# Kernel tuning notes

Hardware: AMD Instinct MI355X
Metric: run time of the kernel (lower is better)

The kernel has to match this reference:

```python
import jax, jax.numpy as jnp
import numpy as np
from jax import lax

V_PATCH = (1, 4, 16, 64, 256, 1024)  # must end at L
RESI = 0.5    # quant_resi ratio inside Phi
BETA = 0.25
K_PHI = 4     # share_quant_resi


def _phi_indices():
    # PhiPartiallyShared tick lookup, resolved statically per scale
    K = K_PHI
    ticks = np.linspace(1/3/K, 1 - 1/3/K, K) if K == 4 else np.linspace(1/2/K, 1 - 1/2/K, K)
    SN = len(V_PATCH)
    return [int(np.argmin(np.abs(ticks - (si / (SN - 1) if SN > 1 else 0.0)))) for si in range(SN)]


def interp_linear(x, Lo):
    # torch F.interpolate(mode='linear', align_corners=False) on last axis of [B,C,Li]
    Li = x.shape[-1]
    if Li == Lo:
        return x
    pos = (jnp.arange(Lo, dtype=jnp.float32) + 0.5) * (Li / Lo) - 0.5
    pos = jnp.clip(pos, 0.0, Li - 1)
    lo = jnp.floor(pos).astype(jnp.int32)
    hi = jnp.minimum(lo + 1, Li - 1)
    w = pos - lo.astype(jnp.float32)
    return x[..., lo] * (1.0 - w) + x[..., hi] * w


def phi_apply(h, w, b):
    # Phi: h*(1-r) + Conv1d(ks=3,pad=1)(h)*r
    y = lax.conv_general_dilated(h, w, (1,), [(1, 1)], dimension_numbers=('NCH', 'OIH', 'NCH'))
    y = y + b[None, :, None]
    return h * (1.0 - RESI) + y * RESI


def reference(f_BCL, emb, phi_w, phi_b):
    f = f_BCL.astype(jnp.float32)
    B, C, L = f.shape
    f_ng = lax.stop_gradient(f)
    f_rest = f_ng
    f_hat = jnp.zeros_like(f_ng)
    SN = len(V_PATCH)
    pidx = _phi_indices()
    e_sq = jnp.sum(emb * emb, axis=1)  # [V]
    loss = jnp.float32(0.0)
    for si, pl in enumerate(V_PATCH):
        rest = interp_linear(f_rest, pl) if si != SN - 1 else f_rest
        z = rest.transpose(0, 2, 1).reshape(-1, C)              # [B*pl, C]
        d = jnp.sum(z * z, axis=1, keepdims=True) + e_sq - 2.0 * (z @ emb.T)  # [B*pl, V]
        idx = jnp.argmin(d, axis=1)
        h = emb[idx].reshape(B, pl, C).transpose(0, 2, 1)        # [B,C,pl]
        if si != SN - 1:
            h = interp_linear(h, L)
        h = phi_apply(h, phi_w[pidx[si]], phi_b[pidx[si]])
        f_hat = f_hat + h
        f_rest = f_rest - h
        loss = loss + BETA * jnp.mean((lax.stop_gradient(f_hat) - f) ** 2) \
                    + jnp.mean((f_hat - f_ng) ** 2)
    loss = loss / SN
    # straight-through estimator
    f_hat_st = lax.stop_gradient(f_hat) - f_ng + f
    return f_hat_st, loss


def setup_inputs() -> dict:
    key = jax.random.key(0)
    k1, k2, k3 = jax.random.split(key, 3)
    B, C, L, V = 32, 32, 1024, 4096
    f_BCL = jax.random.normal(k1, (B, C, L), dtype=jnp.float32)
    emb = jax.random.normal(k2, (V, C), dtype=jnp.float32)
    phi_w = jax.random.normal(k3, (K_PHI, C, C, 3), dtype=jnp.float32) * 0.05
    phi_b = jnp.zeros((K_PHI, C), dtype=jnp.float32)
    return {"f_BCL": f_BCL, "emb": emb, "phi_w": phi_w, "phi_b": phi_b}
```

## Files before the change

kernel.cpp:

```cpp
#include <hip/hip_runtime.h>
#include <stdint.h>

#define BDIM 32
#define CDIM 32
#define LDIM 1024
#define VDIM 4096
#define BCL (BDIM*CDIM*LDIM)

typedef _Float16 f16x8 __attribute__((ext_vector_type(8)));
typedef float f32x4 __attribute__((ext_vector_type(4)));

#define PIN_V(x) asm volatile("" : "+v"(x))

__global__ void init_kernel(const float* __restrict__ f, const float* __restrict__ emb,
                            float* __restrict__ f_rest, float* __restrict__ f_hat,
                            float* __restrict__ e_sq,
                            _Float16* __restrict__ eh, _Float16* __restrict__ el,
                            float* __restrict__ loss_acc, unsigned* __restrict__ done_ctr,
                            unsigned long long* __restrict__ keys, int nkeys) {
    int i = blockIdx.x * blockDim.x + threadIdx.x;
    if (i < BCL) { f_rest[i] = f[i]; f_hat[i] = 0.0f; }
    if (i < VDIM) {
        const float* e = emb + (size_t)i * CDIM;
        float s = 0.f;
#pragma unroll
        for (int k = 0; k < 32; ++k) {
            float v = e[k];
            s = fmaf(v, v, s);
            if (eh) {
                _Float16 h = (_Float16)v;
                float r = v - (float)h;
                eh[(size_t)i*32 + k] = (_Float16)(-2.0f) * h;
                el[(size_t)i*32 + k] = (_Float16)(-2.0f) * (_Float16)r;
            }
        }
        e_sq[i] = s;
    }
    if (i < nkeys) keys[i] = ~0ull;
    if (i == 0) { *loss_acc = 0.f; *done_ctr = 0u; }
}

__global__ __launch_bounds__(256) void vq_mfma(
    const _Float16* __restrict__ z_hi, const _Float16* __restrict__ z_lo,
    const _Float16* __restrict__ e_hi, const _Float16* __restrict__ e_lo,
    const float* __restrict__ e_sq, unsigned long long* __restrict__ keys,
    int NQ, int VC, int vchunks, int vsub)
{
    const int t = threadIdx.x;
    const int lane = t & 63;
    const int w = t >> 6;
    const int qg = blockIdx.x / vchunks;
    const int vc = blockIdx.x % vchunks;
    const int vb0 = vc * (vsub * VC);

    __shared__ __align__(16) _Float16 eh_ls[256*32];
    __shared__ __align__(16) _Float16 el_ls[256*32];
    __shared__ float esq_ls[256];

    const int fr = lane & 15;
    const int kq = lane >> 4;
    const int qbase = qg*256 + w*64;
    f16x8 ah[4], al[4];
#pragma unroll
    for (int tq = 0; tq < 4; ++tq) {
        int q = qbase + tq*16 + fr;
        ah[tq] = *(const f16x8*)(z_hi + (size_t)q*32 + kq*8);
        al[tq] = *(const f16x8*)(z_lo + (size_t)q*32 + kq*8);
    }

    float bd[4][4]; int bv[4][4];
#pragma unroll
    for (int tq = 0; tq < 4; ++tq)
#pragma unroll
        for (int i = 0; i < 4; ++i) { bd[tq][i] = 3.4e38f; bv[tq][i] = 0; }

    for (int sub = 0; sub < vsub; ++sub) {
        const int vb = vb0 + sub * VC;

        {
            const float4* sH = (const float4*)(e_hi + (size_t)vb*32);
            const float4* sL = (const float4*)(e_lo + (size_t)vb*32);
            float4* dH = (float4*)eh_ls; float4* dL = (float4*)el_ls;
            int n4 = VC * 4;
            for (int x = t; x < n4; x += 256) {
                int row = x >> 2, c = x & 3;
                int ds = row*4 + (c ^ ((row >> 1) & 3));
                dH[ds] = sH[x]; dL[ds] = sL[x];
            }
            for (int v = t; v < VC; v += 256) esq_ls[v] = e_sq[vb + v];
        }
        __syncthreads();

        for (int vt = 0; vt < VC; vt += 16) {
            const int row = vt + fr;
            const int koff = (kq ^ ((row >> 1) & 3)) * 8;
            const f16x8 bh = *(const f16x8*)(eh_ls + (size_t)row*32 + koff);
            const f16x8 bl = *(const f16x8*)(el_ls + (size_t)row*32 + koff);
            float es = esq_ls[row];
            int vg = vb + row;
#pragma unroll
            for (int tq = 0; tq < 4; ++tq) {
                f32x4 acc = {es, es, es, es};
                acc = __builtin_amdgcn_mfma_f32_16x16x32_f16(ah[tq], bh, acc, 0,0,0);
                acc = __builtin_amdgcn_mfma_f32_16x16x32_f16(ah[tq], bl, acc, 0,0,0);
                acc = __builtin_amdgcn_mfma_f32_16x16x32_f16(al[tq], bh, acc, 0,0,0);
#pragma unroll
                for (int i = 0; i < 4; ++i)
                    if (acc[i] < bd[tq][i]) { bd[tq][i] = acc[i]; bv[tq][i] = vg; }
            }
        }
        __syncthreads();
    }

#pragma unroll
    for (int tq = 0; tq < 4; ++tq) {
#pragma unroll
        for (int i = 0; i < 4; ++i) {
            unsigned u = __float_as_uint(bd[tq][i]);
            u = (u & 0x80000000u) ? ~u : (u | 0x80000000u);
            unsigned long long k = ((unsigned long long)u << 32) | (unsigned)bv[tq][i];
#pragma unroll
            for (int m = 1; m < 16; m <<= 1) {
                unsigned long long o = __shfl_xor(k, m, 64); if (o < k) k = o;
            }
            if (fr == 0) {
                int q = qbase + tq*16 + kq*4 + i;
                atomicMin(&keys[q], k);
            }
        }
    }
}

__global__ __launch_bounds__(256) void vq_scan(
    const float* __restrict__ f_rest, const float* __restrict__ z_buf,
    const float* __restrict__ emb, const float* __restrict__ e_sq,
    unsigned long long* __restrict__ keys,
    int lpl, int s, int NQ, int VC, int vchunks)
{
    const int pl = 1 << lpl;
    const int t  = threadIdx.x;
    const int qg = blockIdx.x / vchunks;
    const int vc = blockIdx.x % vchunks;
    const int vb = vc * VC;

    __shared__ __align__(16) float e_ls[128 * 32];
    __shared__ float esq_ls[128];

    {
        const float4* src = (const float4*)emb + (size_t)vb * 8;
        float4* dst = (float4*)e_ls;
        for (int x = t; x < VC * 8; x += 256) dst[x] = src[x];
        if (t < VC) esq_ls[t] = e_sq[vb + t];
    }

    const int q0 = qg * 512 + t;
    const int q1 = q0 + 256;
    const int qc0 = (q0 < NQ) ? q0 : NQ - 1;
    const int qc1 = (q1 < NQ) ? q1 : NQ - 1;

    float z0[32], z1[32];
    if (z_buf) {
        const float4* p0 = (const float4*)(z_buf + (size_t)qc0 * 32);
        const float4* p1 = (const float4*)(z_buf + (size_t)qc1 * 32);
#pragma unroll
        for (int c4 = 0; c4 < 8; ++c4) {
            float4 a = p0[c4], b = p1[c4];
            z0[c4*4+0] = a.x; z0[c4*4+1] = a.y; z0[c4*4+2] = a.z; z0[c4*4+3] = a.w;
            z1[c4*4+0] = b.x; z1[c4*4+1] = b.y; z1[c4*4+2] = b.z; z1[c4*4+3] = b.w;
        }
    } else {
        int b0 = qc0 >> lpl, j0 = qc0 & (pl - 1);
        int b1 = qc1 >> lpl, j1 = qc1 & (pl - 1);
        if (pl == LDIM) {
            const float* p0 = f_rest + b0 * (CDIM * LDIM) + j0;
            const float* p1 = f_rest + b1 * (CDIM * LDIM) + j1;
#pragma unroll
            for (int c = 0; c < 32; ++c) { z0[c] = p0[c * LDIM]; z1[c] = p1[c * LDIM]; }
        } else {
            int col0 = j0 * s + (s >> 1) - 1;
            int col1 = j1 * s + (s >> 1) - 1;
            const float* p0 = f_rest + b0 * (CDIM * LDIM) + col0;
            const float* p1 = f_rest + b1 * (CDIM * LDIM) + col1;
#pragma unroll
            for (int c = 0; c < 32; ++c) {
                z0[c] = 0.5f * (p0[c * LDIM] + p0[c * LDIM + 1]);
                z1[c] = 0.5f * (p1[c * LDIM] + p1[c * LDIM + 1]);
            }
        }
    }

    __syncthreads();

    float bd0 = 3.4e38f, bd1 = 3.4e38f;
    int bv0 = 0, bv1 = 0;

#pragma unroll 1
    for (int v = 0; v < VC; v += 2) {
#pragma unroll
        for (int c = 0; c < 32; ++c) { PIN_V(z0[c]); PIN_V(z1[c]); }

        const float4* er0 = (const float4*)&e_ls[(size_t)v * 32];
        const float4* er1 = er0 + 8;
        float es0 = esq_ls[v];
        float es1 = esq_ls[v + 1];

        float4 e0 = er0[0], e1 = er1[0];
        float a00 = z0[0] * e0.x,        a01 = z0[0] * e1.x;
        float a10 = z1[0] * e0.x,        a11 = z1[0] * e1.x;
        a00 = fmaf(z0[1], e0.y, a00);    a01 = fmaf(z0[1], e1.y, a01);
        a10 = fmaf(z1[1], e0.y, a10);    a11 = fmaf(z1[1], e1.y, a11);
        a00 = fmaf(z0[2], e0.z, a00);    a01 = fmaf(z0[2], e1.z, a01);
        a10 = fmaf(z1[2], e0.z, a10);    a11 = fmaf(z1[2], e1.z, a11);
        a00 = fmaf(z0[3], e0.w, a00);    a01 = fmaf(z0[3], e1.w, a01);
        a10 = fmaf(z1[3], e0.w, a10);    a11 = fmaf(z1[3], e1.w, a11);
#pragma unroll
        for (int c4 = 1; c4 < 8; ++c4) {
            e0 = er0[c4]; e1 = er1[c4];
            a00 = fmaf(z0[c4*4+0], e0.x, a00);  a01 = fmaf(z0[c4*4+0], e1.x, a01);
            a10 = fmaf(z1[c4*4+0], e0.x, a10);  a11 = fmaf(z1[c4*4+0], e1.x, a11);
            a00 = fmaf(z0[c4*4+1], e0.y, a00);  a01 = fmaf(z0[c4*4+1], e1.y, a01);
            a10 = fmaf(z1[c4*4+1], e0.y, a10);  a11 = fmaf(z1[c4*4+1], e1.y, a11);
            a00 = fmaf(z0[c4*4+2], e0.z, a00);  a01 = fmaf(z0[c4*4+2], e1.z, a01);
            a10 = fmaf(z1[c4*4+2], e0.z, a10);  a11 = fmaf(z1[c4*4+2], e1.z, a11);
            a00 = fmaf(z0[c4*4+3], e0.w, a00);  a01 = fmaf(z0[c4*4+3], e1.w, a01);
            a10 = fmaf(z1[c4*4+3], e0.w, a10);  a11 = fmaf(z1[c4*4+3], e1.w, a11);
        }
        float d00 = fmaf(a00, -2.0f, es0);
        float d01 = fmaf(a01, -2.0f, es1);
        float d10 = fmaf(a10, -2.0f, es0);
        float d11 = fmaf(a11, -2.0f, es1);
        if (d00 < bd0) { bd0 = d00; bv0 = vb + v; }
        if (d01 < bd0) { bd0 = d01; bv0 = vb + v + 1; }
        if (d10 < bd1) { bd1 = d10; bv1 = vb + v; }
        if (d11 < bd1) { bd1 = d11; bv1 = vb + v + 1; }
    }

    if (q0 < NQ) {
        unsigned ud = __float_as_uint(bd0);
        ud = (ud & 0x80000000u) ? ~ud : (ud | 0x80000000u);
        atomicMin(&keys[q0], ((unsigned long long)ud << 32) | (unsigned)bv0);
    }
    if (q1 < NQ) {
        unsigned ud = __float_as_uint(bd1);
        ud = (ud & 0x80000000u) ? ~ud : (ud | 0x80000000u);
        atomicMin(&keys[q1], ((unsigned long long)ud << 32) | (unsigned)bv1);
    }
}

__global__ __launch_bounds__(256) void fuse_kernel(
    const float* __restrict__ f, const float* __restrict__ emb,
    const unsigned long long* __restrict__ keys,
    unsigned long long* __restrict__ keys_next, int nq_next,
    _Float16* __restrict__ zh_next, _Float16* __restrict__ zl_next, int s_next,
    const float* __restrict__ w, const float* __restrict__ bias,
    float* __restrict__ f_rest, float* __restrict__ f_hat,
    float* __restrict__ loss_acc, unsigned* __restrict__ done_ctr,
    float* __restrict__ out_loss, int pl)
{
    const int t  = threadIdx.x;
    const int b  = blockIdx.y;
    const int l0 = blockIdx.x * 64;

    if (keys_next) {
        int x = (b * gridDim.x + blockIdx.x) * 256 + t;
        if (x < nq_next) keys_next[x] = ~0ull;
    }

    __shared__ float w_s[3072];
    __shared__ float b_s[32];
    __shared__ float hs[32 * 68];
    __shared__ float red[4];

    for (int x = t; x < 3072; x += 256) w_s[x] = w[x];
    if (t < 32) b_s[t] = bias[t];

    if (t < 66) {
        int l = l0 - 1 + t;
        if (l < 0 || l >= LDIM) {
#pragma unroll
            for (int i = 0; i < 32; ++i) hs[i * 68 + t] = 0.f;
        } else {
            int lo, hi; float wg;
            if (pl == LDIM) { lo = l; hi = l; wg = 0.f; }
            else {
                float pos = (l + 0.5f) * ((float)pl / 1024.0f) - 0.5f;
                pos = fminf(fmaxf(pos, 0.f), (float)(pl - 1));
                lo = (int)floorf(pos);
                hi = min(lo + 1, pl - 1);
                wg = pos - (float)lo;
            }
            int v0 = (int)(keys[b * pl + lo] & 0xFFFFFFFFull);
            int v1 = (int)(keys[b * pl + hi] & 0xFFFFFFFFull);
            const float4* e0 = (const float4*)(emb + (size_t)v0 * 32);
            const float4* e1 = (const float4*)(emb + (size_t)v1 * 32);
            float om = 1.0f - wg;
#pragma unroll
            for (int i4 = 0; i4 < 8; ++i4) {
                float4 a = e0[i4]; float4 c = e1[i4];
                hs[(i4*4+0) * 68 + t] = a.x * om + c.x * wg;
                hs[(i4*4+1) * 68 + t] = a.y * om + c.y * wg;
                hs[(i4*4+2) * 68 + t] = a.z * om + c.z * wg;
                hs[(i4*4+3) * 68 + t] = a.w * om + c.w * wg;
            }
        }
    }
    __syncthreads();

    const int o  = t >> 3;
    const int lg = t & 7;
    const float* wrow = &w_s[o * 96];
    float acc[8];
#pragma unroll
    for (int u = 0; u < 8; ++u) acc[u] = 0.f;
    const int hbase = lg * 8;

    for (int i = 0; i < 32; ++i) {
        float w0 = wrow[i * 3 + 0], w1 = wrow[i * 3 + 1], w2 = wrow[i * 3 + 2];
        const float* hrow = &hs[i * 68 + hbase];
        float hw[10];
#pragma unroll
        for (int x = 0; x < 10; ++x) hw[x] = hrow[x];
#pragma unroll
        for (int u = 0; u < 8; ++u) {
            acc[u] = fmaf(w0, hw[u], acc[u]);
            acc[u] = fmaf(w1, hw[u + 1], acc[u]);
            acc[u] = fmaf(w2, hw[u + 2], acc[u]);
        }
    }

    float lsum = 0.f;
    float frv[8];
    const int gbase = (b * 32 + o) * LDIM + l0 + lg * 8;
#pragma unroll
    for (int u = 0; u < 8; ++u) {
        float hval = hs[o * 68 + lg * 8 + 1 + u];
        float y = acc[u] + b_s[o];
        float ph = 0.5f * hval + 0.5f * y;
        int gi = gbase + u;
        float fh = f_hat[gi] + ph;
        f_hat[gi] = fh;
        float fr = f_rest[gi] - ph;
        f_rest[gi] = fr;
        frv[u] = fr;
        float df = fh - f[gi];
        lsum = fmaf(df, df, lsum);
    }

    if (zh_next) {
        __syncthreads();
#pragma unroll
        for (int u = 0; u < 8; ++u) hs[o * 68 + lg * 8 + u] = frv[u];
        __syncthreads();
        int npos = 64 / s_next;
        int qn_base = b * (LDIM / s_next) + l0 / s_next;
        for (int v = t; v < npos * 32; v += 256) {
            int jl = v >> 5, c = v & 31;
            float zv;
            if (s_next == 1) zv = hs[c * 68 + jl];
            else {
                int cl = jl * s_next + (s_next >> 1) - 1;
                zv = 0.5f * (hs[c * 68 + cl] + hs[c * 68 + cl + 1]);
            }
            _Float16 h = (_Float16)zv;
            float r = zv - (float)h;
            size_t zi = (size_t)(qn_base + jl) * 32 + c;
            zh_next[zi] = h;
            zl_next[zi] = (_Float16)r;
        }
    }

#pragma unroll
    for (int off = 32; off > 0; off >>= 1) lsum += __shfl_down(lsum, off, 64);
    if ((t & 63) == 0) red[t >> 6] = lsum;
    __syncthreads();
    if (t == 0) {
        atomicAdd(loss_acc, red[0] + red[1] + red[2] + red[3]);
        if (out_loss) {
            __threadfence();
            unsigned old = atomicAdd(done_ctr, 1u);
            if (old == (unsigned)(gridDim.x * gridDim.y - 1)) {
                float lv = atomicAdd(loss_acc, 0.0f);
                *out_loss = lv * (1.25f / (6.0f * (float)BCL));
            }
        }
    }
}

extern "C" void kernel_launch(void* const* d_in, const int* in_sizes, int n_in,
                              void* d_out, int out_size, void* d_ws, size_t ws_size,
                              hipStream_t stream)
{
    const float* f    = (const float*)d_in[0];
    const float* emb  = (const float*)d_in[1];
    const float* phiw = (const float*)d_in[2];
    const float* phib = (const float*)d_in[3];

    float* f_hat    = (float*)d_out;
    float* out_loss = f_hat + BCL;

    const int pls[6]   = {1, 4, 16, 64, 256, 1024};
    const int lpls[6]  = {0, 2, 4, 6, 8, 10};
    const int vch[6]   = {64, 64, 64, 64, 32, 32};
    const int vchm[6]  = {0, 0, 64, 16, 8, 4};
    const int vsbm[6]  = {0, 0, 1, 1, 2, 4};
    const int pidx[6]  = {0, 0, 1, 2, 3, 3};
    const int snx[6]   = {256, 64, 16, 4, 1, 0};

    char* ws = (char*)d_ws;
    float* f_rest = (float*)ws;

    size_t base = (size_t)BCL * 4;
    size_t off = base;
    unsigned long long* keysA = (unsigned long long*)(ws + off);
    unsigned long long* keysB = keysA + 32768;
    off += (size_t)65536 * 8;
    _Float16* z_hi = (_Float16*)(ws + off); off += (size_t)32768 * 32 * 2;
    _Float16* z_lo = (_Float16*)(ws + off); off += (size_t)32768 * 32 * 2;
    _Float16* e_hi = (_Float16*)(ws + off); off += (size_t)VDIM * 32 * 2;
    _Float16* e_lo = (_Float16*)(ws + off); off += (size_t)VDIM * 32 * 2;
    size_t need_mf = off + (size_t)VDIM * 4 + 64;
    bool mf = ws_size >= need_mf;

    if (!mf) {
        off = base;
        size_t need_pp = base + (size_t)65536 * 8 + (size_t)VDIM * 4 + 64;
        bool pp = ws_size >= need_pp;
        keysB = pp ? keysA + 32768 : keysA;
        off += pp ? (size_t)65536 * 8 : (size_t)32768 * 8;
        float* e_sq        = (float*)(ws + off);
        float* loss_acc    = e_sq + VDIM;
        unsigned* done_ctr = (unsigned*)(loss_acc + 1);

        init_kernel<<<dim3((BCL + 255) / 256), 256, 0, stream>>>(
            f, emb, f_rest, f_hat, e_sq, nullptr, nullptr, loss_acc, done_ctr, keysA, 32768);

        for (int si = 0; si < 6; ++si) {
            int pl = pls[si], s = LDIM / pl, NQ = BDIM * pl;
            int qgroups = (NQ + 511) >> 9;
            int VC = VDIM / vch[si];
            unsigned long long* k  = (si & 1) ? keysB : keysA;
            unsigned long long* kn = (si < 5 && pp) ? ((si & 1) ? keysA : keysB) : nullptr;
            int nq_next = (si < 5) ? BDIM * pls[si + 1] : 0;
            if (!pp && si > 0) hipMemsetAsync(k, 0xFF, (size_t)NQ * 8, stream);
            vq_scan<<<dim3(qgroups * vch[si]), 256, 0, stream>>>(
                f_rest, nullptr, emb, e_sq, k, lpls[si], s, NQ, VC, vch[si]);
            fuse_kernel<<<dim3(16, 32), 256, 0, stream>>>(
                f, emb, k, kn, nq_next, nullptr, nullptr, snx[si],
                phiw + (size_t)pidx[si] * 3072, phib + (size_t)pidx[si] * 32,
                f_rest, f_hat, loss_acc, done_ctr,
                (si == 5) ? out_loss : nullptr, pl);
        }
        return;
    }

    float* e_sq        = (float*)(ws + off);
    float* loss_acc    = e_sq + VDIM;
    unsigned* done_ctr = (unsigned*)(loss_acc + 1);

    init_kernel<<<dim3((BCL + 255) / 256), 256, 0, stream>>>(
        f, emb, f_rest, f_hat, e_sq, e_hi, e_lo, loss_acc, done_ctr, keysA, 32768);

    for (int si = 0; si < 6; ++si) {
        int pl = pls[si], s = LDIM / pl, NQ = BDIM * pl;
        unsigned long long* k  = (si & 1) ? keysB : keysA;
        unsigned long long* kn = (si < 5) ? ((si & 1) ? keysA : keysB) : nullptr;
        int nq_next = (si < 5) ? BDIM * pls[si + 1] : 0;
        if (si >= 2) {
            int vcm = vchm[si], vsb = vsbm[si];
            int VC = VDIM / (vcm * vsb);
            vq_mfma<<<dim3((NQ / 256) * vcm), 256, 0, stream>>>(
                z_hi, z_lo, e_hi, e_lo, e_sq, k, NQ, VC, vcm, vsb);
        } else {
            int qgroups = (NQ + 511) >> 9;
            vq_scan<<<dim3(qgroups * vch[si]), 256, 0, stream>>>(
                f_rest, nullptr, emb, e_sq, k, lpls[si], s, NQ, VDIM / vch[si], vch[si]);
        }
        bool zw = (si >= 1 && si <= 4);
        fuse_kernel<<<dim3(16, 32), 256, 0, stream>>>(
            f, emb, k, kn, nq_next,
            zw ? z_hi : nullptr, zw ? z_lo : nullptr, snx[si],
            phiw + (size_t)pidx[si] * 3072, phib + (size_t)pidx[si] * 32,
            f_rest, f_hat, loss_acc, done_ctr,
            (si == 5) ? out_loss : nullptr, pl);
    }
}
```

Measured before the change: 321.1 us.

## Fuse all VQ scales into one cooperative persistent kernel with grid syncs

Replaces the 13-launch sequence (init plus scan and fuse per scale) with a single cooperative kernel of 512 blocks that runs every phase and separates them with grid.sync(). Scale 0 and 1 now use a per-query parallel scan split across threads, and scales 2-3 use a staged fp32 scan over the hi/lo z buffers. The aim is to remove launch overhead and inter-kernel gaps on a chain of many small kernels. The trade-offs are grid-wide barrier cost, fixed occupancy of 512 blocks, a shared-memory union that may limit residency, and a fallback to the old path if the cooperative launch fails.

Measured after the change: 929.2 us. +189.4%, slower.

```diff
diff --git a/kernel.cpp b/kernel.cpp
--- a/kernel.cpp
+++ b/kernel.cpp
@@ -1,5 +1,8 @@
 #include <hip/hip_runtime.h>
+#include <hip/hip_cooperative_groups.h>
 #include <stdint.h>
+
+namespace cg = cooperative_groups;
 
 #define BDIM 32
 #define CDIM 32
@@ -11,6 +14,367 @@
 typedef float f32x4 __attribute__((ext_vector_type(4)));
 
 #define PIN_V(x) asm volatile("" : "+v"(x))
+
+__device__ __forceinline__ unsigned long long pack_key(float bd, int bv) {
+    unsigned u = __float_as_uint(bd);
+    u = (u & 0x80000000u) ? ~u : (u | 0x80000000u);
+    return ((unsigned long long)u << 32) | (unsigned)bv;
+}
+
+struct __align__(16) SmemVQ { _Float16 eh[256*32]; _Float16 el[256*32]; float esq[256]; };
+struct SmemFU { float w_s[3072]; float b_s[32]; float hs[32*68]; float red[4]; };
+union SmemU { SmemVQ vq; SmemFU fu; };
+
+__device__ void pair_scan(int lpl, int s, int NQ, const float* __restrict__ f_rest,
+                          const float* __restrict__ emb, const float* __restrict__ e_sq,
+                          unsigned long long* __restrict__ keys, int gtid, int t)
+{
+    const int pl = 1 << lpl;
+    const int tpq = 131072 / NQ;
+    const int nv = VDIM / tpq;
+    const int q = gtid / tpq;
+    const int vstart = (gtid % tpq) * nv;
+    int b = q >> lpl, j = q & (pl - 1);
+    int col = j * s + (s >> 1) - 1;
+    const float* p = f_rest + b * (CDIM * LDIM) + col;
+    float z[32];
+#pragma unroll
+    for (int c = 0; c < 32; ++c) z[c] = 0.5f * (p[c * LDIM] + p[c * LDIM + 1]);
+    float bd = 3.4e38f; int bv = 0;
+    for (int v = vstart; v < vstart + nv; ++v) {
+        const float* e = emb + (size_t)v * 32;
+        float es = e_sq[v];
+        float a = z[0] * e[0];
+#pragma unroll
+        for (int c = 1; c < 32; ++c) a = fmaf(z[c], e[c], a);
+        float d = fmaf(a, -2.0f, es);
+        if (d < bd) { bd = d; bv = v; }
+    }
+    unsigned long long key = pack_key(bd, bv);
+#pragma unroll
+    for (int m = 1; m < 64; m <<= 1) {
+        unsigned long long o = __shfl_xor(key, m, 64); if (o < key) key = o;
+    }
+    __shared__ unsigned long long redk[4];
+    if ((t & 63) == 0) redk[t >> 6] = key;
+    __syncthreads();
+    if (t == 0) {
+        unsigned long long kk = redk[0];
+#pragma unroll
+        for (int m = 1; m < 4; ++m) if (redk[m] < kk) kk = redk[m];
+        atomicMin(&keys[q], kk);
+    }
+    __syncthreads();
+}
+
+__device__ void staged_scan(int NQ, const _Float16* __restrict__ z_hi,
+                            const _Float16* __restrict__ z_lo,
+                            const float* __restrict__ emb, const float* __restrict__ e_sq,
+                            unsigned long long* __restrict__ keys,
+                            int bid, int t, SmemVQ& smv)
+{
+    const int qgroups = NQ >> 8;
+    const int vchunks = 64;
+    if (bid >= qgroups * vchunks) return;
+    const int qg = bid / vchunks, vc = bid % vchunks;
+    const int VC = 64;
+    const int vb = vc * VC;
+    float* e_s   = (float*)smv.eh;
+    float* esq_s = smv.esq;
+    {
+        const float4* src = (const float4*)(emb + (size_t)vb * 32);
+        float4* dst = (float4*)e_s;
+        for (int x = t; x < VC * 8; x += 256) dst[x] = src[x];
+        if (t < VC) esq_s[t] = e_sq[vb + t];
+    }
+    const int q = qg * 256 + t;
+    const _Float16* zh = z_hi + (size_t)q * 32;
+    const _Float16* zl = z_lo + (size_t)q * 32;
+    float z[32];
+#pragma unroll
+    for (int c = 0; c < 32; ++c) z[c] = (float)zh[c] + (float)zl[c];
+    __syncthreads();
+    float bd = 3.4e38f; int bv = 0;
+    for (int v = 0; v < VC; ++v) {
+        const float* e = e_s + v * 32;
+        float es = esq_s[v];
+        float a = z[0] * e[0];
+#pragma unroll
+        for (int c = 1; c < 32; ++c) a = fmaf(z[c], e[c], a);
+        float d = fmaf(a, -2.0f, es);
+        if (d < bd) { bd = d; bv = vb + v; }
+    }
+    atomicMin(&keys[q], pack_key(bd, bv));
+}
+
+__device__ void mfma_phase(const _Float16* __restrict__ z_hi, const _Float16* __restrict__ z_lo,
+                           const _Float16* __restrict__ e_hi, const _Float16* __restrict__ e_lo,
+                           const float* __restrict__ e_sq, unsigned long long* __restrict__ keys,
+                           int NQ, int VC, int vchunks, int vsub,
+                           int bid, int t, SmemVQ& smv)
+{
+    const int lane = t & 63;
+    const int w = t >> 6;
+    const int qg = bid / vchunks;
+    const int vc = bid % vchunks;
+    const int vb0 = vc * (vsub * VC);
+
+    const int fr = lane & 15;
+    const int kq = lane >> 4;
+    const int qbase = qg * 256 + w * 64;
+    f16x8 ah[4], al[4];
+#pragma unroll
+    for (int tq = 0; tq < 4; ++tq) {
+        int q = qbase + tq * 16 + fr;
+        ah[tq] = *(const f16x8*)(z_hi + (size_t)q * 32 + kq * 8);
+        al[tq] = *(const f16x8*)(z_lo + (size_t)q * 32 + kq * 8);
+    }
+
+    float bd[4][4]; int bv[4][4];
+#pragma unroll
+    for (int tq = 0; tq < 4; ++tq)
+#pragma unroll
+        for (int i = 0; i < 4; ++i) { bd[tq][i] = 3.4e38f; bv[tq][i] = 0; }
+
+    for (int sub = 0; sub < vsub; ++sub) {
+        const int vb = vb0 + sub * VC;
+        {
+            const float4* sH = (const float4*)(e_hi + (size_t)vb * 32);
+            const float4* sL = (const float4*)(e_lo + (size_t)vb * 32);
+            float4* dH = (float4*)smv.eh; float4* dL = (float4*)smv.el;
+            int n4 = VC * 4;
+            for (int x = t; x < n4; x += 256) {
+                int row = x >> 2, c = x & 3;
+                int ds = row * 4 + (c ^ ((row >> 1) & 3));
+                dH[ds] = sH[x]; dL[ds] = sL[x];
+            }
+            for (int v = t; v < VC; v += 256) smv.esq[v] = e_sq[vb + v];
+        }
+        __syncthreads();
+
+        for (int vt = 0; vt < VC; vt += 16) {
+            const int row = vt + fr;
+            const int koff = (kq ^ ((row >> 1) & 3)) * 8;
+            const f16x8 bh = *(const f16x8*)(smv.eh + (size_t)row * 32 + koff);
+            const f16x8 bl = *(const f16x8*)(smv.el + (size_t)row * 32 + koff);
+            float es = smv.esq[row];
+            int vg = vb + row;
+#pragma unroll
+            for (int tq = 0; tq < 4; ++tq) {
+                f32x4 acc = {es, es, es, es};
+                acc = __builtin_amdgcn_mfma_f32_16x16x32_f16(ah[tq], bh, acc, 0,0,0);
+                acc = __builtin_amdgcn_mfma_f32_16x16x32_f16(ah[tq], bl, acc, 0,0,0);
+                acc = __builtin_amdgcn_mfma_f32_16x16x32_f16(al[tq], bh, acc, 0,0,0);
+#pragma unroll
+                for (int i = 0; i < 4; ++i)
+                    if (acc[i] < bd[tq][i]) { bd[tq][i] = acc[i]; bv[tq][i] = vg; }
+            }
+        }
+        __syncthreads();
+    }
+
+#pragma unroll
+    for (int tq = 0; tq < 4; ++tq) {
+#pragma unroll
+        for (int i = 0; i < 4; ++i) {
+            unsigned long long k = pack_key(bd[tq][i], bv[tq][i]);
+#pragma unroll
+            for (int m = 1; m < 16; m <<= 1) {
+                unsigned long long o = __shfl_xor(k, m, 64); if (o < k) k = o;
+            }
+            if (fr == 0) atomicMin(&keys[qbase + tq * 16 + kq * 4 + i], k);
+        }
+    }
+}
+
+__device__ void fuse_phase(const float* __restrict__ f, const float* __restrict__ emb,
+                           const unsigned long long* __restrict__ keys,
+                           unsigned long long* __restrict__ keys_next, int nq_next,
+                           _Float16* __restrict__ zh_next, _Float16* __restrict__ zl_next,
+                           int s_next, const float* __restrict__ w, const float* __restrict__ bias,
+                           float* __restrict__ f_rest, float* __restrict__ f_hat,
+                           float* __restrict__ loss_acc, int pl,
+                           int bid, int t, SmemFU& smf)
+{
+    const int b  = bid >> 4;
+    const int l0 = (bid & 15) * 64;
+
+    if (keys_next) {
+        int x = bid * 256 + t;
+        if (x < nq_next) keys_next[x] = ~0ull;
+    }
+
+    for (int x = t; x < 3072; x += 256) smf.w_s[x] = w[x];
+    if (t < 32) smf.b_s[t] = bias[t];
+
+    if (t < 66) {
+        int l = l0 - 1 + t;
+        if (l < 0 || l >= LDIM) {
+#pragma unroll
+            for (int i = 0; i < 32; ++i) smf.hs[i * 68 + t] = 0.f;
+        } else {
+            int lo, hi; float wg;
+            if (pl == LDIM) { lo = l; hi = l; wg = 0.f; }
+            else {
+                float pos = (l + 0.5f) * ((float)pl / 1024.0f) - 0.5f;
+                pos = fminf(fmaxf(pos, 0.f), (float)(pl - 1));
+                lo = (int)floorf(pos);
+                hi = min(lo + 1, pl - 1);
+                wg = pos - (float)lo;
+            }
+            int v0 = (int)(keys[b * pl + lo] & 0xFFFFFFFFull);
+            int v1 = (int)(keys[b * pl + hi] & 0xFFFFFFFFull);
+            const float4* e0 = (const float4*)(emb + (size_t)v0 * 32);
+            const float4* e1 = (const float4*)(emb + (size_t)v1 * 32);
+            float om = 1.0f - wg;
+#pragma unroll
+            for (int i4 = 0; i4 < 8; ++i4) {
+                float4 a = e0[i4]; float4 c = e1[i4];
+                smf.hs[(i4*4+0) * 68 + t] = a.x * om + c.x * wg;
+                smf.hs[(i4*4+1) * 68 + t] = a.y * om + c.y * wg;
+                smf.hs[(i4*4+2) * 68 + t] = a.z * om + c.z * wg;
+                smf.hs[(i4*4+3) * 68 + t] = a.w * om + c.w * wg;
+            }
+        }
+    }
+    __syncthreads();
+
+    const int o  = t >> 3;
+    const int lg = t & 7;
+    const float* wrow = &smf.w_s[o * 96];
+    float acc[8];
+#pragma unroll
+    for (int u = 0; u < 8; ++u) acc[u] = 0.f;
+    const int hbase = lg * 8;
+
+    for (int i = 0; i < 32; ++i) {
+        float w0 = wrow[i * 3 + 0], w1 = wrow[i * 3 + 1], w2 = wrow[i * 3 + 2];
+        const float* hrow = &smf.hs[i * 68 + hbase];
+        float hw[10];
+#pragma unroll
+        for (int x = 0; x < 10; ++x) hw[x] = hrow[x];
+#pragma unroll
+        for (int u = 0; u < 8; ++u) {
+            acc[u] = fmaf(w0, hw[u], acc[u]);
+            acc[u] = fmaf(w1, hw[u + 1], acc[u]);
+            acc[u] = fmaf(w2, hw[u + 2], acc[u]);
+        }
+    }
+
+    float lsum = 0.f;
+    float frv[8];
+    const int gbase = (b * 32 + o) * LDIM + l0 + lg * 8;
+#pragma unroll
+    for (int u = 0; u < 8; ++u) {
+        float hval = smf.hs[o * 68 + lg * 8 + 1 + u];
+        float y = acc[u] + smf.b_s[o];
+        float ph = 0.5f * hval + 0.5f * y;
+        int gi = gbase + u;
+        float fh = f_hat[gi] + ph;
+        f_hat[gi] = fh;
+        float fr = f_rest[gi] - ph;
+        f_rest[gi] = fr;
+        frv[u] = fr;
+        float df = fh - f[gi];
+        lsum = fmaf(df, df, lsum);
+    }
+
+    if (zh_next) {
+        __syncthreads();
+#pragma unroll
+        for (int u = 0; u < 8; ++u) smf.hs[o * 68 + lg * 8 + u] = frv[u];
+        __syncthreads();
+        int npos = 64 / s_next;
+        int qn_base = b * (LDIM / s_next) + l0 / s_next;
+        for (int v = t; v < npos * 32; v += 256) {
+            int jl = v >> 5, c = v & 31;
+            float zv;
+            if (s_next == 1) zv = smf.hs[c * 68 + jl];
+            else {
+                int cl = jl * s_next + (s_next >> 1) - 1;
+                zv = 0.5f * (smf.hs[c * 68 + cl] + smf.hs[c * 68 + cl + 1]);
+            }
+            _Float16 h = (_Float16)zv;
+            float r = zv - (float)h;
+            size_t zi = (size_t)(qn_base + jl) * 32 + c;
+            zh_next[zi] = h;
+            zl_next[zi] = (_Float16)r;
+        }
+    }
+
+#pragma unroll
+    for (int off = 32; off > 0; off >>= 1) lsum += __shfl_down(lsum, off, 64);
+    if ((t & 63) == 0) smf.red[t >> 6] = lsum;
+    __syncthreads();
+    if (t == 0) atomicAdd(loss_acc, smf.red[0] + smf.red[1] + smf.red[2] + smf.red[3]);
+}
+
+__global__ __launch_bounds__(256) void mega(
+    const float* __restrict__ f, const float* __restrict__ emb,
+    const float* __restrict__ phiw, const float* __restrict__ phib,
+    float* __restrict__ f_hat, float* __restrict__ out_loss,
+    float* __restrict__ f_rest,
+    unsigned long long* __restrict__ keysA, unsigned long long* __restrict__ keysB,
+    _Float16* __restrict__ z_hi, _Float16* __restrict__ z_lo,
+    _Float16* __restrict__ e_hi, _Float16* __restrict__ e_lo,
+    float* __restrict__ e_sq, float* __restrict__ loss_acc)
+{
+    __shared__ SmemU sm;
+    cg::grid_group grid = cg::this_grid();
+    const int bid = blockIdx.x, t = threadIdx.x;
+    const int gtid = bid * 256 + t;
+
+    {
+        const float4* f4 = (const float4*)f;
+        float4* fr4 = (float4*)f_rest;
+        float4* fh4 = (float4*)f_hat;
+        float4 zz = make_float4(0.f, 0.f, 0.f, 0.f);
+        for (int i = gtid; i < BCL / 4; i += 131072) { fr4[i] = f4[i]; fh4[i] = zz; }
+        if (gtid < VDIM) {
+            const float* e = emb + (size_t)gtid * 32;
+            float ssum = 0.f;
+#pragma unroll
+            for (int k = 0; k < 32; ++k) {
+                float v = e[k];
+                ssum = fmaf(v, v, ssum);
+                _Float16 h = (_Float16)v;
+                float r = v - (float)h;
+                e_hi[(size_t)gtid*32 + k] = (_Float16)(-2.0f) * h;
+                e_lo[(size_t)gtid*32 + k] = (_Float16)(-2.0f) * (_Float16)r;
+            }
+            e_sq[gtid] = ssum;
+        }
+        if (gtid < 32768) keysA[gtid] = ~0ull;
+        if (gtid == 0) *loss_acc = 0.f;
+    }
+    grid.sync();
+
+    const int pls[6]  = {1, 4, 16, 64, 256, 1024};
+    const int lpls[6] = {0, 2, 4, 6, 8, 10};
+    const int pidx[6] = {0, 0, 1, 2, 3, 3};
+    const int snxv[6] = {256, 64, 16, 4, 1, 0};
+
+    for (int si = 0; si < 6; ++si) {
+        unsigned long long* k  = (si & 1) ? keysB : keysA;
+        unsigned long long* kn = (si & 1) ? keysA : keysB;
+        int pl = pls[si], s = LDIM / pl, NQ = BDIM * pl;
+
+        if (si <= 1)      pair_scan(lpls[si], s, NQ, f_rest, emb, e_sq, k, gtid, t);
+        else if (si <= 3) staged_scan(NQ, z_hi, z_lo, emb, e_sq, k, bid, t, sm.vq);
+        else if (si == 4) mfma_phase(z_hi, z_lo, e_hi, e_lo, e_sq, k, NQ, 256, 16, 1, bid, t, sm.vq);
+        else              mfma_phase(z_hi, z_lo, e_hi, e_lo, e_sq, k, NQ, 256, 4, 4, bid, t, sm.vq);
+        grid.sync();
+
+        bool zw = (si >= 1 && si <= 4);
+        fuse_phase(f, emb, k, (si < 5) ? kn : nullptr, (si < 5) ? BDIM * pls[si + 1] : 0,
+                   zw ? z_hi : nullptr, zw ? z_lo : nullptr, snxv[si],
+                   phiw + (size_t)pidx[si] * 3072, phib + (size_t)pidx[si] * 32,
+                   f_rest, f_hat, loss_acc, pl, bid, t, sm.fu);
+        grid.sync();
+    }
+
+    if (gtid == 0) *out_loss = (*loss_acc) * (1.25f / (6.0f * (float)BCL));
+}
 
 __global__ void init_kernel(const float* __restrict__ f, const float* __restrict__ emb,
                             float* __restrict__ f_rest, float* __restrict__ f_hat,
@@ -46,89 +410,9 @@
     const float* __restrict__ e_sq, unsigned long long* __restrict__ keys,
     int NQ, int VC, int vchunks, int vsub)
 {
-    const int t = threadIdx.x;
-    const int lane = t & 63;
-    const int w = t >> 6;
-    const int qg = blockIdx.x / vchunks;
-    const int vc = blockIdx.x % vchunks;
-    const int vb0 = vc * (vsub * VC);
-
-    __shared__ __align__(16) _Float16 eh_ls[256*32];
-    __shared__ __align__(16) _Float16 el_ls[256*32];
-    __shared__ float esq_ls[256];
-
-    const int fr = lane & 15;
-    const int kq = lane >> 4;
-    const int qbase = qg*256 + w*64;
-    f16x8 ah[4], al[4];
-#pragma unroll
-    for (int tq = 0; tq < 4; ++tq) {
-        int q = qbase + tq*16 + fr;
-        ah[tq] = *(const f16x8*)(z_hi + (size_t)q*32 + kq*8);
-        al[tq] = *(const f16x8*)(z_lo + (size_t)q*32 + kq*8);
-    }
-
-    float bd[4][4]; int bv[4][4];
-#pragma unroll
-    for (int tq = 0; tq < 4; ++tq)
-#pragma unroll
-        for (int i = 0; i < 4; ++i) { bd[tq][i] = 3.4e38f; bv[tq][i] = 0; }
-
-    for (int sub = 0; sub < vsub; ++sub) {
-        const int vb = vb0 + sub * VC;
-
-        {
-            const float4* sH = (const float4*)(e_hi + (size_t)vb*32);
-            const float4* sL = (const float4*)(e_lo + (size_t)vb*32);
-            float4* dH = (float4*)eh_ls; float4* dL = (float4*)el_ls;
-            int n4 = VC * 4;
-            for (int x = t; x < n4; x += 256) {
-                int row = x >> 2, c = x & 3;
-                int ds = row*4 + (c ^ ((row >> 1) & 3));
-                dH[ds] = sH[x]; dL[ds] = sL[x];
-            }
-            for (int v = t; v < VC; v += 256) esq_ls[v] = e_sq[vb + v];
-        }
-        __syncthreads();
-
-        for (int vt = 0; vt < VC; vt += 16) {
-            const int row = vt + fr;
-            const int koff = (kq ^ ((row >> 1) & 3)) * 8;
-            const f16x8 bh = *(const f16x8*)(eh_ls + (size_t)row*32 + koff);
-            const f16x8 bl = *(const f16x8*)(el_ls + (size_t)row*32 + koff);
-            float es = esq_ls[row];
-            int vg = vb + row;
-#pragma unroll
-            for (int tq = 0; tq < 4; ++tq) {
-                f32x4 acc = {es, es, es, es};
-                acc = __builtin_amdgcn_mfma_f32_16x16x32_f16(ah[tq], bh, acc, 0,0,0);
-                acc = __builtin_amdgcn_mfma_f32_16x16x32_f16(ah[tq], bl, acc, 0,0,0);
-                acc = __builtin_amdgcn_mfma_f32_16x16x32_f16(al[tq], bh, acc, 0,0,0);
-#pragma unroll
-                for (int i = 0; i < 4; ++i)
-                    if (acc[i] < bd[tq][i]) { bd[tq][i] = acc[i]; bv[tq][i] = vg; }
-            }
-        }
-        __syncthreads();
-    }
-
-#pragma unroll
-    for (int tq = 0; tq < 4; ++tq) {
-#pragma unroll
-        for (int i = 0; i < 4; ++i) {
-            unsigned u = __float_as_uint(bd[tq][i]);
-            u = (u & 0x80000000u) ? ~u : (u | 0x80000000u);
-            unsigned long long k = ((unsigned long long)u << 32) | (unsigned)bv[tq][i];
-#pragma unroll
-            for (int m = 1; m < 16; m <<= 1) {
-                unsigned long long o = __shfl_xor(k, m, 64); if (o < k) k = o;
-            }
-            if (fr == 0) {
-                int q = qbase + tq*16 + kq*4 + i;
-                atomicMin(&keys[q], k);
-            }
-        }
-    }
+    __shared__ SmemVQ smv;
+    mfma_phase(z_hi, z_lo, e_hi, e_lo, e_sq, keys, NQ, VC, vchunks, vsub,
+               blockIdx.x, threadIdx.x, smv);
 }
 
 __global__ __launch_bounds__(256) void vq_scan(
@@ -159,16 +443,7 @@
     const int qc1 = (q1 < NQ) ? q1 : NQ - 1;
 
     float z0[32], z1[32];
-    if (z_buf) {
-        const float4* p0 = (const float4*)(z_buf + (size_t)qc0 * 32);
-        const float4* p1 = (const float4*)(z_buf + (size_t)qc1 * 32);
-#pragma unroll
-        for (int c4 = 0; c4 < 8; ++c4) {
-            float4 a = p0[c4], b = p1[c4];
-            z0[c4*4+0] = a.x; z0[c4*4+1] = a.y; z0[c4*4+2] = a.z; z0[c4*4+3] = a.w;
-            z1[c4*4+0] = b.x; z1[c4*4+1] = b.y; z1[c4*4+2] = b.z; z1[c4*4+3] = b.w;
-        }
-    } else {
+    {
         int b0 = qc0 >> lpl, j0 = qc0 & (pl - 1);
         int b1 = qc1 >> lpl, j1 = qc1 & (pl - 1);
         if (pl == LDIM) {
@@ -235,16 +510,8 @@
         if (d11 < bd1) { bd1 = d11; bv1 = vb + v + 1; }
     }
 
-    if (q0 < NQ) {
-        unsigned ud = __float_as_uint(bd0);
-        ud = (ud & 0x80000000u) ? ~ud : (ud | 0x80000000u);
-        atomicMin(&keys[q0], ((unsigned long long)ud << 32) | (unsigned)bv0);
-    }
-    if (q1 < NQ) {
-        unsigned ud = __float_as_uint(bd1);
-        ud = (ud & 0x80000000u) ? ~ud : (ud | 0x80000000u);
-        atomicMin(&keys[q1], ((unsigned long long)ud << 32) | (unsigned)bv1);
-    }
+    if (q0 < NQ) atomicMin(&keys[q0], pack_key(bd0, bv0));
+    if (q1 < NQ) atomicMin(&keys[q1], pack_key(bd1, bv1));
 }
 
 __global__ __launch_bounds__(256) void fuse_kernel(
@@ -257,131 +524,16 @@
     float* __restrict__ loss_acc, unsigned* __restrict__ done_ctr,
     float* __restrict__ out_loss, int pl)
 {
-    const int t  = threadIdx.x;
-    const int b  = blockIdx.y;
-    const int l0 = blockIdx.x * 64;
-
-    if (keys_next) {
-        int x = (b * gridDim.x + blockIdx.x) * 256 + t;
-        if (x < nq_next) keys_next[x] = ~0ull;
-    }
-
-    __shared__ float w_s[3072];
-    __shared__ float b_s[32];
-    __shared__ float hs[32 * 68];
-    __shared__ float red[4];
-
-    for (int x = t; x < 3072; x += 256) w_s[x] = w[x];
-    if (t < 32) b_s[t] = bias[t];
-
-    if (t < 66) {
-        int l = l0 - 1 + t;
-        if (l < 0 || l >= LDIM) {
-#pragma unroll
-            for (int i = 0; i < 32; ++i) hs[i * 68 + t] = 0.f;
-        } else {
-            int lo, hi; float wg;
-            if (pl == LDIM) { lo = l; hi = l; wg = 0.f; }
-            else {
-                float pos = (l + 0.5f) * ((float)pl / 1024.0f) - 0.5f;
-                pos = fminf(fmaxf(pos, 0.f), (float)(pl - 1));
-                lo = (int)floorf(pos);
-                hi = min(lo + 1, pl - 1);
-                wg = pos - (float)lo;
-            }
-            int v0 = (int)(keys[b * pl + lo] & 0xFFFFFFFFull);
-            int v1 = (int)(keys[b * pl + hi] & 0xFFFFFFFFull);
-            const float4* e0 = (const float4*)(emb + (size_t)v0 * 32);
-            const float4* e1 = (const float4*)(emb + (size_t)v1 * 32);
-            float om = 1.0f - wg;
-#pragma unroll
-            for (int i4 = 0; i4 < 8; ++i4) {
-                float4 a = e0[i4]; float4 c = e1[i4];
-                hs[(i4*4+0) * 68 + t] = a.x * om + c.x * wg;
-                hs[(i4*4+1) * 68 + t] = a.y * om + c.y * wg;
-                hs[(i4*4+2) * 68 + t] = a.z * om + c.z * wg;
-                hs[(i4*4+3) * 68 + t] = a.w * om + c.w * wg;
-            }
-        }
-    }
-    __syncthreads();
-
-    const int o  = t >> 3;
-    const int lg = t & 7;
-    const float* wrow = &w_s[o * 96];
-    float acc[8];
-#pragma unroll
-    for (int u = 0; u < 8; ++u) acc[u] = 0.f;
-    const int hbase = lg * 8;
-
-    for (int i = 0; i < 32; ++i) {
-        float w0 = wrow[i * 3 + 0], w1 = wrow[i * 3 + 1], w2 = wrow[i * 3 + 2];
-        const float* hrow = &hs[i * 68 + hbase];
-        float hw[10];
-#pragma unroll
-        for (int x = 0; x < 10; ++x) hw[x] = hrow[x];
-#pragma unroll
-        for (int u = 0; u < 8; ++u) {
-            acc[u] = fmaf(w0, hw[u], acc[u]);
-            acc[u] = fmaf(w1, hw[u + 1], acc[u]);
-            acc[u] = fmaf(w2, hw[u + 2], acc[u]);
-        }
-    }
-
-    float lsum = 0.f;
-    float frv[8];
-    const int gbase = (b * 32 + o) * LDIM + l0 + lg * 8;
-#pragma unroll
-    for (int u = 0; u < 8; ++u) {
-        float hval = hs[o * 68 + lg * 8 + 1 + u];
-        float y = acc[u] + b_s[o];
-        float ph = 0.5f * hval + 0.5f * y;
-        int gi = gbase + u;
-        float fh = f_hat[gi] + ph;
-        f_hat[gi] = fh;
-        float fr = f_rest[gi] - ph;
-        f_rest[gi] = fr;
-        frv[u] = fr;
-        float df = fh - f[gi];
-        lsum = fmaf(df, df, lsum);
-    }
-
-    if (zh_next) {
-        __syncthreads();
-#pragma unroll
-        for (int u = 0; u < 8; ++u) hs[o * 68 + lg * 8 + u] = frv[u];
-        __syncthreads();
-        int npos = 64 / s_next;
-        int qn_base = b * (LDIM / s_next) + l0 / s_next;
-        for (int v = t; v < npos * 32; v += 256) {
-            int jl = v >> 5, c = v & 31;
-            float zv;
-            if (s_next == 1) zv = hs[c * 68 + jl];
-            else {
-                int cl = jl * s_next + (s_next >> 1) - 1;
-                zv = 0.5f * (hs[c * 68 + cl] + hs[c * 68 + cl + 1]);
-            }
-            _Float16 h = (_Float16)zv;
-            float r = zv - (float)h;
-            size_t zi = (size_t)(qn_base + jl) * 32 + c;
-            zh_next[zi] = h;
-            zl_next[zi] = (_Float16)r;
-        }
-    }
-
-#pragma unroll
-    for (int off = 32; off > 0; off >>= 1) lsum += __shfl_down(lsum, off, 64);
-    if ((t & 63) == 0) red[t >> 6] = lsum;
-    __syncthreads();
-    if (t == 0) {
-        atomicAdd(loss_acc, red[0] + red[1] + red[2] + red[3]);
-        if (out_loss) {
-            __threadfence();
-            unsigned old = atomicAdd(done_ctr, 1u);
-            if (old == (unsigned)(gridDim.x * gridDim.y - 1)) {
-                float lv = atomicAdd(loss_acc, 0.0f);
-                *out_loss = lv * (1.25f / (6.0f * (float)BCL));
-            }
+    __shared__ SmemFU smf;
+    int bid = blockIdx.y * gridDim.x + blockIdx.x;
+    fuse_phase(f, emb, keys, keys_next, nq_next, zh_next, zl_next, s_next,
+               w, bias, f_rest, f_hat, loss_acc, pl, bid, threadIdx.x, smf);
+    if (threadIdx.x == 0 && out_loss) {
+        __threadfence();
+        unsigned old = atomicAdd(done_ctr, 1u);
+        if (old == (unsigned)(gridDim.x * gridDim.y - 1)) {
+            float lv = atomicAdd(loss_acc, 0.0f);
+            *out_loss = lv * (1.25f / (6.0f * (float)BCL));
         }
     }
 }
@@ -421,7 +573,55 @@
     size_t need_mf = off + (size_t)VDIM * 4 + 64;
     bool mf = ws_size >= need_mf;
 
-    if (!mf) {
+    if (mf) {
+        float* e_sq        = (float*)(ws + off);
+        float* loss_acc    = e_sq + VDIM;
+        unsigned* done_ctr = (unsigned*)(loss_acc + 1);
+
+        {
+            void* kargs[] = {
+                (void*)&f, (void*)&emb, (void*)&phiw, (void*)&phib,
+                (void*)&f_hat, (void*)&out_loss, (void*)&f_rest,
+                (void*)&keysA, (void*)&keysB, (void*)&z_hi, (void*)&z_lo,
+                (void*)&e_hi, (void*)&e_lo, (void*)&e_sq, (void*)&loss_acc
+            };
+            hipError_t err = hipLaunchCooperativeKernel(
+                reinterpret_cast<const void*>(&mega), dim3(512), dim3(256),
+                kargs, 0, stream);
+            if (err == hipSuccess) return;
+            (void)hipGetLastError();
+        }
+
+        init_kernel<<<dim3((BCL + 255) / 256), 256, 0, stream>>>(
+            f, emb, f_rest, f_hat, e_sq, e_hi, e_lo, loss_acc, done_ctr, keysA, 32768);
+
+        for (int si = 0; si < 6; ++si) {
+            int pl = pls[si], s = LDIM / pl, NQ = BDIM * pl;
+            unsigned long long* k  = (si & 1) ? keysB : keysA;
+            unsigned long long* kn = (si < 5) ? ((si & 1) ? keysA : keysB) : nullptr;
+            int nq_next = (si < 5) ? BDIM * pls[si + 1] : 0;
+            if (si >= 2) {
+                int vcm = vchm[si], vsb = vsbm[si];
+                int VC = VDIM / (vcm * vsb);
+                vq_mfma<<<dim3((NQ / 256) * vcm), 256, 0, stream>>>(
+                    z_hi, z_lo, e_hi, e_lo, e_sq, k, NQ, VC, vcm, vsb);
+            } else {
+                int qgroups = (NQ + 511) >> 9;
+                vq_scan<<<dim3(qgroups * vch[si]), 256, 0, stream>>>(
+                    f_rest, nullptr, emb, e_sq, k, lpls[si], s, NQ, VDIM / vch[si], vch[si]);
+            }
+            bool zw = (si >= 1 && si <= 4);
+            fuse_kernel<<<dim3(16, 32), 256, 0, stream>>>(
+                f, emb, k, kn, nq_next,
+                zw ? z_hi : nullptr, zw ? z_lo : nullptr, snx[si],
+                phiw + (size_t)pidx[si] * 3072, phib + (size_t)pidx[si] * 32,
+                f_rest, f_hat, loss_acc, done_ctr,
+                (si == 5) ? out_loss : nullptr, pl);
+        }
+        return;
+    }
+
+    {
         off = base;
         size_t need_pp = base + (size_t)65536 * 8 + (size_t)VDIM * 4 + 64;
         bool pp = ws_size >= need_pp;
@@ -450,37 +650,5 @@
                 f_rest, f_hat, loss_acc, done_ctr,
                 (si == 5) ? out_loss : nullptr, pl);
         }
-        return;
-    }
-
-    float* e_sq        = (float*)(ws + off);
-    float* loss_acc    = e_sq + VDIM;
-    unsigned* done_ctr = (unsigned*)(loss_acc + 1);
-
-    init_kernel<<<dim3((BCL + 255) / 256), 256, 0, stream>>>(
-        f, emb, f_rest, f_hat, e_sq, e_hi, e_lo, loss_acc, done_ctr, keysA, 32768);
-
-    for (int si = 0; si < 6; ++si) {
-        int pl = pls[si], s = LDIM / pl, NQ = BDIM * pl;
-        unsigned long long* k  = (si & 1) ? keysB : keysA;
-        unsigned long long* kn = (si < 5) ? ((si & 1) ? keysA : keysB) : nullptr;
-        int nq_next = (si < 5) ? BDIM * pls[si + 1] : 0;
-        if (si >= 2) {
-            int vcm = vchm[si], vsb = vsbm[si];
-            int VC = VDIM / (vcm * vsb);
-            vq_mfma<<<dim3((NQ / 256) * vcm), 256, 0, stream>>>(
-                z_hi, z_lo, e_hi, e_lo, e_sq, k, NQ, VC, vcm, vsb);
-        } else {
-            int qgroups = (NQ + 511) >> 9;
-            vq_scan<<<dim3(qgroups * vch[si]), 256, 0, stream>>>(
-                f_rest, nullptr, emb, e_sq, k, lpls[si], s, NQ, VDIM / vch[si], vch[si]);
-        }
-        bool zw = (si >= 1 && si <= 4);
-        fuse_kernel<<<dim3(16, 32), 256, 0, stream>>>(
-            f, emb, k, kn, nq_next,
-            zw ? z_hi : nullptr, zw ? z_lo : nullptr, snx[si],
-            phiw + (size_t)pidx[si] * 3072, phib + (size_t)pidx[si] * 32,
-            f_rest, f_hat, loss_acc, done_ctr,
-            (si == 5) ? out_loss : nullptr, pl);
-    }
-}
+    }
+}
```
